# Kernel optimization log

Hardware: AMD Instinct MI355X
Metric: run time of the kernel (lower is better)

## Reference

```python
import jax, jax.numpy as jnp
import numpy as np

B, N, HID = 2, 2048, 1024
NH = 16
HD = HID // NH

def setup_inputs() -> dict:
    key = jax.random.key(0)
    ks = jax.random.split(key, 5)
    s = 0.02
    return {
        "hidden_states": jax.random.normal(ks[0], (B, N, HID), jnp.float32),
        "attention_mask": jnp.zeros((B, 1, 1, N), jnp.float32),
        "Wq": jax.random.normal(ks[1], (HID, HID), jnp.float32) * s,
        "bq": jnp.zeros((HID,), jnp.float32),
        "Wk": jax.random.normal(ks[2], (HID, HID), jnp.float32) * s,
        "bk": jnp.zeros((HID,), jnp.float32),
        "Wv": jax.random.normal(ks[3], (HID, HID), jnp.float32) * s,
        "bv": jnp.zeros((HID,), jnp.float32),
    }

def reference(hidden_states, attention_mask, Wq, bq, Wk, bk, Wv, bv):
    b, n, _ = hidden_states.shape
    def split_heads(t):  # [b,n,hid] -> [b,h,n,d]
        return t.reshape(b, n, NH, HD).transpose(0, 2, 1, 3)
    q = split_heads(hidden_states @ Wq.T + bq)
    k = split_heads(hidden_states @ Wk.T + bk)
    v = split_heads(hidden_states @ Wv.T + bv)
    scores = jnp.einsum('bhnd,bhmd->bhnm', q, k) / jnp.sqrt(jnp.float32(HD)).astype(q.dtype)
    scores = scores + attention_mask
    scores = jnp.maximum(scores, jnp.finfo(scores.dtype).min)
    probs = jax.nn.softmax(scores, axis=-1)
    out = jnp.einsum('bhnm,bhmd->bhnd', probs, v)
    return out.transpose(0, 2, 1, 3).reshape(b, n, NH * HD)
```

## Files before the change

### kernel.cpp

```cpp
#include <hip/hip_runtime.h>

typedef unsigned short u16;
typedef unsigned int   u32;
typedef __attribute__((ext_vector_type(8))) short bf16x8;
typedef __attribute__((ext_vector_type(4))) float f32x4;
typedef __attribute__((ext_vector_type(2))) unsigned int u32x2;

__device__ __forceinline__ float bf2f(u16 u) { return __uint_as_float(((u32)u) << 16); }
__device__ __forceinline__ u16 f2bf(float f) {
    return (u16)((__float_as_uint(f) + 0x8000u) >> 16);
}
__device__ __forceinline__ u32 cvt_pk_bf16(float lo, float hi) {
    u32 r;
    asm("v_cvt_pk_bf16_f32 %0, %1, %2" : "=v"(r) : "v"(lo), "v"(hi));
    return r;
}
__device__ __forceinline__ void gload16(const void* g, void* l) {
    __builtin_amdgcn_global_load_lds((const __attribute__((address_space(1))) void*)g,
                                     (__attribute__((address_space(3))) void*)l, 16, 0, 0);
}

struct us4 { u16 x, y, z, w; };
__global__ void cvt_all(const float* __restrict__ hs, const float* __restrict__ wq,
                        const float* __restrict__ wk, const float* __restrict__ wv,
                        u16* __restrict__ dst)
{
    int i = blockIdx.x * blockDim.x + threadIdx.x;
    const int stride = gridDim.x * blockDim.x;
    us4* d4 = (us4*)dst;
    for (; i < 1835008; i += stride) {
        const float4* s4;
        int j = i;
        if (j < 1048576)      { s4 = (const float4*)hs; }
        else if (j < 1310720) { s4 = (const float4*)wq; j -= 1048576; }
        else if (j < 1572864) { s4 = (const float4*)wk; j -= 1310720; }
        else                  { s4 = (const float4*)wv; j -= 1572864; }
        float4 v = s4[j];
        us4 o;
        o.x = f2bf(v.x); o.y = f2bf(v.y); o.z = f2bf(v.z); o.w = f2bf(v.w);
        d4[i] = o;
    }
}

__global__ __launch_bounds__(256) void qkv_gemm(
    const u16* __restrict__ hs,
    const u16* __restrict__ Wq, const u16* __restrict__ Wk, const u16* __restrict__ Wv,
    const float* __restrict__ bq, const float* __restrict__ bk, const float* __restrict__ bv,
    u16* __restrict__ oq, u16* __restrict__ ok, u16* __restrict__ ovt)
{
    __shared__ u16 smem[12288];
    u16* sA = smem;
    u16* sB = smem + 4096;

    const int tid  = threadIdx.x;
    const int lane = tid & 63;
    const int wv_  = tid >> 6;
    const int c15  = lane & 15;
    const int q4   = lane >> 4;
    const int rb   = blockIdx.x;
    const int mat  = blockIdx.y >> 3;
    const int cb   = blockIdx.y & 7;

    const u16*   W    = (mat == 0) ? Wq : (mat == 1 ? Wk : Wv);
    const float* bias = (mat == 0) ? bq : (mat == 1 ? bk : bv);

    f32x4 acc[4][2] = {};

    int rA[2], cA[2], rB[4], cB[4];
#pragma unroll
    for (int p = 0; p < 2; ++p) {
        const int ch = p * 256 + tid;
        rA[p] = ch >> 3; cA[p] = ((ch & 7) ^ (rA[p] & 7)) * 8;
    }
#pragma unroll
    for (int p = 0; p < 4; ++p) {
        const int ch = p * 256 + tid;
        rB[p] = ch >> 3; cB[p] = ((ch & 7) ^ (rB[p] & 7)) * 8;
    }
    const u16* gA = hs + (rb * 64) * 1024;
    const u16* gB = W + (cb * 128) * 1024;
    const int swz = c15 & 7;

    for (int kb = 0; kb < 1024; kb += 64) {
        __syncthreads();
#pragma unroll
        for (int p = 0; p < 2; ++p)
            gload16(gA + rA[p] * 1024 + kb + cA[p], sA + (p * 256 + wv_ * 64) * 8);
#pragma unroll
        for (int p = 0; p < 4; ++p)
            gload16(gB + rB[p] * 1024 + kb + cB[p], sB + (p * 256 + wv_ * 64) * 8);
        __syncthreads();

#pragma unroll
        for (int kk = 0; kk < 2; ++kk) {
            const int cpos = ((kk * 4 + q4) ^ swz) * 8;
            bf16x8 af[4], bf[2];
#pragma unroll
            for (int mt = 0; mt < 4; ++mt)
                af[mt] = *(const bf16x8*)(sA + (mt * 16 + c15) * 64 + cpos);
#pragma unroll
            for (int nt = 0; nt < 2; ++nt)
                bf[nt] = *(const bf16x8*)(sB + (wv_ * 32 + nt * 16 + c15) * 64 + cpos);
#pragma unroll
            for (int mt = 0; mt < 4; ++mt)
#pragma unroll
                for (int nt = 0; nt < 2; ++nt)
                    acc[mt][nt] = __builtin_amdgcn_mfma_f32_16x16x32_bf16(
                        af[mt], bf[nt], acc[mt][nt], 0, 0, 0);
        }
    }

    __syncthreads();
    const int hcol = cb * 2 + (wv_ >> 1);
    const int dbase = (wv_ & 1) * 32;
    float bvv[2];
#pragma unroll
    for (int nt = 0; nt < 2; ++nt)
        bvv[nt] = bias[cb * 128 + wv_ * 32 + nt * 16 + c15];

    u16* sc = smem + wv_ * 2560;
    if (mat != 2) {
        u16* dst = (mat == 0) ? oq : ok;
#pragma unroll
        for (int mt = 0; mt < 4; ++mt)
#pragma unroll
            for (int nt = 0; nt < 2; ++nt)
#pragma unroll
                for (int r = 0; r < 4; ++r)
                    sc[(mt * 16 + q4 * 4 + r) * 40 + nt * 16 + c15] =
                        f2bf(acc[mt][nt][r] + bvv[nt]);
#pragma unroll
        for (int i = 0; i < 4; ++i) {
            const int rl = i * 16 + (lane >> 2);
            const int c0 = (lane & 3) * 8;
            bf16x8 vv = *(const bf16x8*)(sc + rl * 40 + c0);
            const int n = rb * 64 + rl;
            const int bb = n >> 11, nn = n & 2047;
            *(bf16x8*)(dst + (((bb * 16 + hcol) * 2048) + nn) * 64 + dbase + c0) = vv;
        }
    } else {
#pragma unroll
        for (int mt = 0; mt < 4; ++mt)
#pragma unroll
            for (int nt = 0; nt < 2; ++nt)
#pragma unroll
                for (int r = 0; r < 4; ++r)
                    sc[(nt * 16 + c15) * 72 + mt * 16 + q4 * 4 + r] =
                        f2bf(acc[mt][nt][r] + bvv[nt]);
#pragma unroll
        for (int i = 0; i < 4; ++i) {
            const int dp = i * 8 + (lane >> 3);
            const int nl = (lane & 7) * 8;
            bf16x8 vv = *(const bf16x8*)(sc + dp * 72 + nl);
            const int n = rb * 64 + nl;
            const int bb = n >> 11, nn = n & 2047;
            *(bf16x8*)(ovt + (((bb * 16 + hcol) * 64) + dbase + dp) * 2048 + nn) = vv;
        }
    }
}

__global__ __launch_bounds__(256, 2) void attn(
    const u16* __restrict__ qm, const u16* __restrict__ km, const u16* __restrict__ vtm,
    const float* __restrict__ mask, float* __restrict__ out)
{
    __shared__ u16 sK0[4096];
    __shared__ u16 sV0[4096];
    __shared__ u16 sK1[4096];
    __shared__ u16 sV1[4096];

    const int tid = threadIdx.x, lane = tid & 63, w = tid >> 6;
    const int c15 = lane & 15, q4 = lane >> 4;
    const int qt = blockIdx.x;
    const int bh = blockIdx.y;
    const int b = bh >> 4;

    bf16x8 qf[2][2];
    const u16* qbase = qm + (bh * 2048 + qt * 128 + w * 32) * 64;
#pragma unroll
    for (int rt = 0; rt < 2; ++rt)
#pragma unroll
        for (int kt = 0; kt < 2; ++kt)
            qf[rt][kt] = *(const bf16x8*)(qbase + (rt * 16 + c15) * 64 + kt * 32 + q4 * 8);

    float l_acc[2] = {0.f, 0.f};
    f32x4 accO[2][4] = {};

    const u16* kbase  = km  + bh * 2048 * 64;
    const u16* vtbase = vtm + bh * 64 * 2048;

    const int row0 = tid >> 3;
    const int col  = ((tid & 7) ^ (row0 & 7)) * 8;
    const int pr0  = (row0 & 0x23) | ((row0 & 0x0C) << 1) | ((row0 & 0x10) >> 2);
    const int kOff0 = pr0 * 64 + col;
    const int kOff1 = kOff0 + 32 * 64;
    const int vOff0 = row0 * 2048 + col;
    const int vOff1 = vOff0 + 32 * 2048;
    const int ldsOff0 = (w * 64) * 8;
    const int ldsOff1 = (256 + w * 64) * 8;

    const float* mbase = mask + b * 2048 + 8 * q4;

    auto compute = [&](const u16* sK, const u16* sVT, int kb) {
        float mkv[4][4];
#pragma unroll
        for (int t = 0; t < 4; ++t) {
            float4 m4 = *(const float4*)(mbase + kb + 32 * (t >> 1) + 4 * (t & 1));
            mkv[t][0] = m4.x * 1.4426950408889634f;
            mkv[t][1] = m4.y * 1.4426950408889634f;
            mkv[t][2] = m4.z * 1.4426950408889634f;
            mkv[t][3] = m4.w * 1.4426950408889634f;
        }

        f32x4 accST[4][2] = {};
#pragma unroll
        for (int kt = 0; kt < 2; ++kt) {
            bf16x8 kf[4];
#pragma unroll
            for (int t = 0; t < 4; ++t) {
                const int rho = t * 16 + c15;
                const int cpos = (kt * 4 + q4) ^ (rho & 7);
                kf[t] = *(const bf16x8*)(sK + rho * 64 + cpos * 8);
            }
#pragma unroll
            for (int t = 0; t < 4; ++t)
#pragma unroll
                for (int rt = 0; rt < 2; ++rt)
                    accST[t][rt] = __builtin_amdgcn_mfma_f32_16x16x32_bf16(
                        kf[t], qf[rt][kt], accST[t][rt], 0, 0, 0);
        }

        u32 pu[4][2][2];
#pragma unroll
        for (int t = 0; t < 4; ++t)
#pragma unroll
            for (int rt = 0; rt < 2; ++rt) {
                float p[4];
#pragma unroll
                for (int rr = 0; rr < 4; ++rr) {
                    p[rr] = __builtin_amdgcn_exp2f(
                        fmaf(accST[t][rt][rr], 0.18033688011112042f, mkv[t][rr]));
                    l_acc[rt] += p[rr];
                }
                pu[t][rt][0] = cvt_pk_bf16(p[0], p[1]);
                pu[t][rt][1] = cvt_pk_bf16(p[2], p[3]);
            }

#pragma unroll
        for (int g = 0; g < 2; ++g) {
            bf16x8 vB[4];
#pragma unroll
            for (int nt = 0; nt < 4; ++nt) {
                const int d = nt * 16 + c15;
                const int pc = (4 * g + q4) ^ (d & 7);
                vB[nt] = *(const bf16x8*)(sVT + d * 64 + pc * 8);
            }
#pragma unroll
            for (int rt = 0; rt < 2; ++rt) {
                union { bf16x8 v; u32 u[4]; } ta;
                ta.u[0] = pu[2 * g][rt][0];
                ta.u[1] = pu[2 * g][rt][1];
                ta.u[2] = pu[2 * g + 1][rt][0];
                ta.u[3] = pu[2 * g + 1][rt][1];
#pragma unroll
                for (int nt = 0; nt < 4; ++nt)
                    accO[rt][nt] = __builtin_amdgcn_mfma_f32_16x16x32_bf16(
                        ta.v, vB[nt], accO[rt][nt], 0, 0, 0);
            }
        }
    };

    gload16(kbase + kOff0, sK0 + ldsOff0);
    gload16(kbase + kOff1, sK0 + ldsOff1);
    gload16(vtbase + vOff0, sV0 + ldsOff0);
    gload16(vtbase + vOff1, sV0 + ldsOff1);
    __syncthreads();

#pragma unroll 1
    for (int it = 0; it < 32; it += 2) {
        {
            const int kb = (it + 1) * 64;
            gload16(kbase + kb * 64 + kOff0, sK1 + ldsOff0);
            gload16(kbase + kb * 64 + kOff1, sK1 + ldsOff1);
            gload16(vtbase + kb + vOff0, sV1 + ldsOff0);
            gload16(vtbase + kb + vOff1, sV1 + ldsOff1);
        }
        compute(sK0, sV0, it * 64);
        __syncthreads();

        if (it + 2 < 32) {
            const int kb = (it + 2) * 64;
            gload16(kbase + kb * 64 + kOff0, sK0 + ldsOff0);
            gload16(kbase + kb * 64 + kOff1, sK0 + ldsOff1);
            gload16(vtbase + kb + vOff0, sV0 + ldsOff0);
            gload16(vtbase + kb + vOff1, sV0 + ldsOff1);
        }
        compute(sK1, sV1, (it + 1) * 64);
        __syncthreads();
    }

#pragma unroll
    for (int rt = 0; rt < 2; ++rt) {
        l_acc[rt] += __shfl_xor(l_acc[rt], 16);
        l_acc[rt] += __shfl_xor(l_acc[rt], 32);
    }

    const int h = bh & 15;
#pragma unroll
    for (int rt = 0; rt < 2; ++rt) {
        float inv[4];
#pragma unroll
        for (int rr = 0; rr < 4; ++rr)
            inv[rr] = 1.0f / __shfl(l_acc[rt], q4 * 4 + rr);
#pragma unroll
        for (int nt = 0; nt < 4; ++nt)
#pragma unroll
            for (int rr = 0; rr < 4; ++rr) {
                const int qrow = qt * 128 + w * 32 + rt * 16 + q4 * 4 + rr;
                const int d = nt * 16 + c15;
                out[(b * 2048 + qrow) * 1024 + h * 64 + d] = accO[rt][nt][rr] * inv[rr];
            }
    }
}

extern "C" void kernel_launch(void* const* d_in, const int* in_sizes, int n_in,
                              void* d_out, int out_size, void* d_ws, size_t ws_size,
                              hipStream_t stream)
{
    const float* hs   = (const float*)d_in[0];
    const float* mask = (const float*)d_in[1];
    const float* Wq   = (const float*)d_in[2];
    const float* bq   = (const float*)d_in[3];
    const float* Wk   = (const float*)d_in[4];
    const float* bk   = (const float*)d_in[5];
    const float* Wv   = (const float*)d_in[6];
    const float* bv   = (const float*)d_in[7];

    u16* ws   = (u16*)d_ws;
    u16* qw   = ws;
    u16* kw   = ws + 4194304;
    u16* vtw  = ws + 8388608;
    u16* hsb  = ws + 12582912;
    u16* wqb  = ws + 16777216;
    u16* wkb  = ws + 17825792;
    u16* wvb  = ws + 18874368;

    cvt_all<<<1024, 256, 0, stream>>>(hs, Wq, Wk, Wv, hsb);

    qkv_gemm<<<dim3(64, 24), 256, 0, stream>>>(hsb, wqb, wkb, wvb, bq, bk, bv, qw, kw, vtw);
    attn<<<dim3(16, 32), 256, 0, stream>>>(qw, kw, vtw, mask, (float*)d_out);
}
```

Baseline: 177.9 us.

## Stage 128-key tiles with vmcnt-gated double buffering and swap grid order

The attention kernel now loads 128-key K/V tiles per stage, twice the previous size. It replaces __syncthreads with explicit vmcnt waits plus raw barriers, so the prefetch of the next tile can stay in flight while the current one is computed. MFMA sections are wrapped in s_setprio to favour the matrix work, and both the GEMM and attention grids swap x/y so that blocks sharing K/V or weights are scheduled adjacently, which should help L2 reuse. LDS per block doubles to 64KB, which may limit occupancy, and the manual waitcnt counts must match the number of outstanding loads.

Result: faster. 166.0 us (-6.7%).

```diff
diff --git a/kernel.cpp b/kernel.cpp
--- a/kernel.cpp
+++ b/kernel.cpp
@@ -19,6 +19,7 @@
     __builtin_amdgcn_global_load_lds((const __attribute__((address_space(1))) void*)g,
                                      (__attribute__((address_space(3))) void*)l, 16, 0, 0);
 }
+#define VMCNT(n) asm volatile("s_waitcnt vmcnt(" #n ")" ::: "memory")
 
 struct us4 { u16 x, y, z, w; };
 __global__ void cvt_all(const float* __restrict__ hs, const float* __restrict__ wq,
@@ -57,9 +58,9 @@
     const int wv_  = tid >> 6;
     const int c15  = lane & 15;
     const int q4   = lane >> 4;
-    const int rb   = blockIdx.x;
-    const int mat  = blockIdx.y >> 3;
-    const int cb   = blockIdx.y & 7;
+    const int rb   = blockIdx.y;
+    const int mat  = blockIdx.x >> 3;
+    const int cb   = blockIdx.x & 7;
 
     const u16*   W    = (mat == 0) ? Wq : (mat == 1 ? Wk : Wv);
     const float* bias = (mat == 0) ? bq : (mat == 1 ? bk : bv);
@@ -163,15 +164,15 @@
     const u16* __restrict__ qm, const u16* __restrict__ km, const u16* __restrict__ vtm,
     const float* __restrict__ mask, float* __restrict__ out)
 {
-    __shared__ u16 sK0[4096];
-    __shared__ u16 sV0[4096];
-    __shared__ u16 sK1[4096];
-    __shared__ u16 sV1[4096];
+    __shared__ u16 sK0[8192];
+    __shared__ u16 sV0[8192];
+    __shared__ u16 sK1[8192];
+    __shared__ u16 sV1[8192];
 
     const int tid = threadIdx.x, lane = tid & 63, w = tid >> 6;
     const int c15 = lane & 15, q4 = lane >> 4;
-    const int qt = blockIdx.x;
-    const int bh = blockIdx.y;
+    const int bh = blockIdx.x;
+    const int qt = blockIdx.y;
     const int b = bh >> 4;
 
     bf16x8 qf[2][2];
@@ -188,19 +189,27 @@
     const u16* kbase  = km  + bh * 2048 * 64;
     const u16* vtbase = vtm + bh * 64 * 2048;
 
-    const int row0 = tid >> 3;
-    const int col  = ((tid & 7) ^ (row0 & 7)) * 8;
-    const int pr0  = (row0 & 0x23) | ((row0 & 0x0C) << 1) | ((row0 & 0x10) >> 2);
-    const int kOff0 = pr0 * 64 + col;
-    const int kOff1 = kOff0 + 32 * 64;
-    const int vOff0 = row0 * 2048 + col;
-    const int vOff1 = vOff0 + 32 * 2048;
-    const int ldsOff0 = (w * 64) * 8;
-    const int ldsOff1 = (256 + w * 64) * 8;
+    const int rK   = tid >> 3;
+    const int colK = ((tid & 7) ^ (rK & 7)) * 8;
+    const int prK  = (rK & 3) | ((rK & 0x0C) << 1) | ((rK & 0x10) >> 2);
+    const int rV   = tid >> 4;
+    const int colV = ((tid & 15) ^ (rV & 7)) * 8;
+    const int ldsW = w * 512;
 
     const float* mbase = mask + b * 2048 + 8 * q4;
 
-    auto compute = [&](const u16* sK, const u16* sVT, int kb) {
+    auto stage = [&](u16* dK, u16* dV, int TT) {
+        const u16* kg = kbase + TT * 128 * 64;
+        const u16* vg = vtbase + TT * 128;
+#pragma unroll
+        for (int p = 0; p < 4; ++p)
+            gload16(kg + (prK + 32 * p) * 64 + colK, dK + p * 2048 + ldsW);
+#pragma unroll
+        for (int p = 0; p < 4; ++p)
+            gload16(vg + (rV + 16 * p) * 2048 + colV, dV + p * 2048 + ldsW);
+    };
+
+    auto compute64 = [&](const u16* sKh, const u16* sVb, int pcBase, int kb) {
         float mkv[4][4];
 #pragma unroll
         for (int t = 0; t < 4; ++t) {
@@ -212,14 +221,14 @@
         }
 
         f32x4 accST[4][2] = {};
+        __builtin_amdgcn_s_setprio(1);
 #pragma unroll
         for (int kt = 0; kt < 2; ++kt) {
             bf16x8 kf[4];
 #pragma unroll
             for (int t = 0; t < 4; ++t) {
-                const int rho = t * 16 + c15;
-                const int cpos = (kt * 4 + q4) ^ (rho & 7);
-                kf[t] = *(const bf16x8*)(sK + rho * 64 + cpos * 8);
+                const int cpos = (kt * 4 + q4) ^ (c15 & 7);
+                kf[t] = *(const bf16x8*)(sKh + (t * 16 + c15) * 64 + cpos * 8);
             }
 #pragma unroll
             for (int t = 0; t < 4; ++t)
@@ -228,6 +237,7 @@
                     accST[t][rt] = __builtin_amdgcn_mfma_f32_16x16x32_bf16(
                         kf[t], qf[rt][kt], accST[t][rt], 0, 0, 0);
         }
+        __builtin_amdgcn_s_setprio(0);
 
         u32 pu[4][2][2];
 #pragma unroll
@@ -245,14 +255,15 @@
                 pu[t][rt][1] = cvt_pk_bf16(p[2], p[3]);
             }
 
+        __builtin_amdgcn_s_setprio(1);
 #pragma unroll
         for (int g = 0; g < 2; ++g) {
             bf16x8 vB[4];
 #pragma unroll
             for (int nt = 0; nt < 4; ++nt) {
                 const int d = nt * 16 + c15;
-                const int pc = (4 * g + q4) ^ (d & 7);
-                vB[nt] = *(const bf16x8*)(sVT + d * 64 + pc * 8);
+                const int pc = pcBase + ((4 * g + q4) ^ (d & 7));
+                vB[nt] = *(const bf16x8*)(sVb + d * 128 + pc * 8);
             }
 #pragma unroll
             for (int rt = 0; rt < 2; ++rt) {
@@ -267,36 +278,42 @@
                         ta.v, vB[nt], accO[rt][nt], 0, 0, 0);
             }
         }
+        __builtin_amdgcn_s_setprio(0);
     };
 
-    gload16(kbase + kOff0, sK0 + ldsOff0);
-    gload16(kbase + kOff1, sK0 + ldsOff1);
-    gload16(vtbase + vOff0, sV0 + ldsOff0);
-    gload16(vtbase + vOff1, sV0 + ldsOff1);
-    __syncthreads();
+    stage(sK0, sV0, 0);
+    stage(sK1, sV1, 1);
 
 #pragma unroll 1
-    for (int it = 0; it < 32; it += 2) {
-        {
-            const int kb = (it + 1) * 64;
-            gload16(kbase + kb * 64 + kOff0, sK1 + ldsOff0);
-            gload16(kbase + kb * 64 + kOff1, sK1 + ldsOff1);
-            gload16(vtbase + kb + vOff0, sV1 + ldsOff0);
-            gload16(vtbase + kb + vOff1, sV1 + ldsOff1);
-        }
-        compute(sK0, sV0, it * 64);
-        __syncthreads();
-
-        if (it + 2 < 32) {
-            const int kb = (it + 2) * 64;
-            gload16(kbase + kb * 64 + kOff0, sK0 + ldsOff0);
-            gload16(kbase + kb * 64 + kOff1, sK0 + ldsOff1);
-            gload16(vtbase + kb + vOff0, sV0 + ldsOff0);
-            gload16(vtbase + kb + vOff1, sV0 + ldsOff1);
-        }
-        compute(sK1, sV1, (it + 1) * 64);
-        __syncthreads();
-    }
+    for (int T = 0; T < 14; T += 2) {
+        VMCNT(8);
+        __builtin_amdgcn_s_barrier();
+        __builtin_amdgcn_sched_barrier(0);
+        compute64(sK0, sV0, 0, T * 128);
+        compute64(sK0 + 64 * 64, sV0, 8, T * 128 + 64);
+        __builtin_amdgcn_s_barrier();
+        __builtin_amdgcn_sched_barrier(0);
+        stage(sK0, sV0, T + 2);
+
+        VMCNT(8);
+        __builtin_amdgcn_s_barrier();
+        __builtin_amdgcn_sched_barrier(0);
+        compute64(sK1, sV1, 0, (T + 1) * 128);
+        compute64(sK1 + 64 * 64, sV1, 8, (T + 1) * 128 + 64);
+        __builtin_amdgcn_s_barrier();
+        __builtin_amdgcn_sched_barrier(0);
+        stage(sK1, sV1, T + 3);
+    }
+    VMCNT(8);
+    __builtin_amdgcn_s_barrier();
+    __builtin_amdgcn_sched_barrier(0);
+    compute64(sK0, sV0, 0, 14 * 128);
+    compute64(sK0 + 64 * 64, sV0, 8, 14 * 128 + 64);
+    VMCNT(0);
+    __builtin_amdgcn_s_barrier();
+    __builtin_amdgcn_sched_barrier(0);
+    compute64(sK1, sV1, 0, 15 * 128);
+    compute64(sK1 + 64 * 64, sV1, 8, 15 * 128 + 64);
 
 #pragma unroll
     for (int rt = 0; rt < 2; ++rt) {
@@ -346,6 +363,6 @@
 
     cvt_all<<<1024, 256, 0, stream>>>(hs, Wq, Wk, Wv, hsb);
 
-    qkv_gemm<<<dim3(64, 24), 256, 0, stream>>>(hsb, wqb, wkb, wvb, bq, bk, bv, qw, kw, vtw);
-    attn<<<dim3(16, 32), 256, 0, stream>>>(qw, kw, vtw, mask, (float*)d_out);
-}
+    qkv_gemm<<<dim3(24, 64), 256, 0, stream>>>(hsb, wqb, wkb, wvb, bq, bk, bv, qw, kw, vtw);
+    attn<<<dim3(32, 16), 256, 0, stream>>>(qw, kw, vtw, mask, (float*)d_out);
+}
```
